# Performance work log

Hardware: AMD Instinct MI355X
Metric: run time of the kernel (lower is better)

Reference implementation:

```python
import jax, jax.numpy as jnp
import numpy as np

B, S, V, NB = 4, 2048, 50257, 32
TEMPERATURE = 0.07
TAU = 1.0  # F.gumbel_softmax default tau


def setup_inputs() -> dict:
    key = jax.random.key(0)
    k_ids, k_proto, k_gumbel = jax.random.split(key, 3)
    token_ids = jax.random.randint(k_ids, (B, S), 0, V)
    onehot_tokens = jax.nn.one_hot(token_ids, V, dtype=jnp.float32)  # [B,S,V]
    prototypes = jax.random.normal(k_proto, (NB, V), dtype=jnp.float32)
    # Gumbel(0,1) noise, pre-sampled so the reference is deterministic
    u = jax.random.uniform(k_gumbel, (B, S, NB), dtype=jnp.float32,
                           minval=1e-20, maxval=1.0)
    gumbel_noise = -jnp.log(-jnp.log(u))
    return {"onehot_tokens": onehot_tokens, "prototypes": prototypes,
            "gumbel_noise": gumbel_noise}


def reference(onehot_tokens, prototypes, gumbel_noise):
    # sims = onehot @ prototypes.T  (functionally a row gather) -> [B,S,NB]
    sims = jnp.einsum("bsv,nv->bsn", onehot_tokens, prototypes)
    logits = sims / TEMPERATURE
    # gumbel_softmax(hard=True): soft probs then straight-through hard one-hot
    y_soft = jax.nn.softmax((logits + gumbel_noise) / TAU, axis=-1)
    idx = jnp.argmax(y_soft, axis=-1)
    y_hard = jax.nn.one_hot(idx, NB, dtype=y_soft.dtype)
    out = y_hard - jax.lax.stop_gradient(y_soft) + y_soft
    return out
```

## Files before the change

kernel.cpp:

```cpp
#include <hip/hip_runtime.h>

#define B_    4
#define S_    2048
#define V_    50257
#define NB_   32
#define BS_   (B_ * S_)
static_assert((long long)BS_ * V_ % 4 == 0, "flat onehot must be float4-divisible");

__global__ __launch_bounds__(256) void find_tokens_kernel(
    const float4* __restrict__ onehot4, long long n4, int* __restrict__ tid)
{
    long long i = (long long)blockIdx.x * blockDim.x + threadIdx.x;
    long long stride = (long long)gridDim.x * blockDim.x;
    for (; i < n4; i += stride) {
        float4 v = onehot4[i];
        if (v.x != 0.0f || v.y != 0.0f || v.z != 0.0f || v.w != 0.0f) {
            long long base = i * 4;
            float vals[4] = {v.x, v.y, v.z, v.w};
            #pragma unroll
            for (int k = 0; k < 4; ++k) {
                if (vals[k] != 0.0f) {
                    long long idx = base + k;
                    int row = (int)(idx / V_);
                    int col = (int)(idx - (long long)row * V_);
                    tid[row] = col;
                }
            }
        }
    }
}

__global__ __launch_bounds__(256) void gumbel_hard_kernel(
    const float* __restrict__ proto,
    const float* __restrict__ gumbel,
    const int*   __restrict__ tid,
    float*       __restrict__ out)
{
    int row = blockIdx.x * blockDim.x + threadIdx.x;
    if (row >= BS_) return;
    int t = tid[row];

    float g[NB_];
    {
        const float4* g4 = reinterpret_cast<const float4*>(gumbel + (long long)row * NB_);
        #pragma unroll
        for (int q = 0; q < NB_ / 4; ++q) {
            float4 v = g4[q];
            g[q * 4 + 0] = v.x; g[q * 4 + 1] = v.y;
            g[q * 4 + 2] = v.z; g[q * 4 + 3] = v.w;
        }
    }

    float z[NB_];
    float m = -1e30f;
    int   am = 0;
    #pragma unroll
    for (int n = 0; n < NB_; ++n) {
        float s = proto[(long long)n * V_ + t];
        float zn = s / 0.07f + g[n];
        z[n] = zn;
        if (zn > m) { m = zn; am = n; }
    }

    float e[NB_];
    float sum = 0.0f;
    #pragma unroll
    for (int n = 0; n < NB_; ++n) {
        e[n] = __expf(z[n] - m);
        sum += e[n];
    }
    float inv = 1.0f / sum;

    float4* o4 = reinterpret_cast<float4*>(out + (long long)row * NB_);
    #pragma unroll
    for (int q = 0; q < NB_ / 4; ++q) {
        float4 v;
        float r[4];
        #pragma unroll
        for (int k = 0; k < 4; ++k) {
            int n = q * 4 + k;
            float y = e[n] * inv;
            float h = (n == am) ? 1.0f : 0.0f;
            r[k] = (h - y) + y;
        }
        v.x = r[0]; v.y = r[1]; v.z = r[2]; v.w = r[3];
        o4[q] = v;
    }
}

extern "C" void kernel_launch(void* const* d_in, const int* in_sizes, int n_in,
                              void* d_out, int out_size, void* d_ws, size_t ws_size,
                              hipStream_t stream)
{
    const float* onehot = (const float*)d_in[0];
    const float* proto  = (const float*)d_in[1];
    const float* gumbel = (const float*)d_in[2];
    float* out = (float*)d_out;
    int* tid = (int*)d_ws;

    long long n4 = ((long long)BS_ * V_) / 4;

    find_tokens_kernel<<<4096, 256, 0, stream>>>(
        reinterpret_cast<const float4*>(onehot), n4, tid);

    gumbel_hard_kernel<<<(BS_ + 255) / 256, 256, 0, stream>>>(
        proto, gumbel, tid, out);
}
```

Measured before the change: 299.9 us.

## Fuse token scan and gumbel-hard emission into a single streaming kernel

Merges the one-hot scan and the per-row softmax/argmax kernels into one kernel: the thread that finds a nonzero element computes and writes that row's output directly, so the tid workspace and the second launch go away. The scan loop is unrolled four-way to keep more loads in flight, the nonzero test uses integer bit checks, and the grid drops from 4096 to 2048 blocks. The emission work becomes divergent inside scanning wavefronts, but it is rare compared with the memory-bound scan of about 1.6 GB.

```diff
diff --git a/kernel.cpp b/kernel.cpp
--- a/kernel.cpp
+++ b/kernel.cpp
@@ -5,41 +5,16 @@
 #define V_    50257
 #define NB_   32
 #define BS_   (B_ * S_)
+#define TEMP_ 0.07f
+
 static_assert((long long)BS_ * V_ % 4 == 0, "flat onehot must be float4-divisible");
 
-__global__ __launch_bounds__(256) void find_tokens_kernel(
-    const float4* __restrict__ onehot4, long long n4, int* __restrict__ tid)
-{
-    long long i = (long long)blockIdx.x * blockDim.x + threadIdx.x;
-    long long stride = (long long)gridDim.x * blockDim.x;
-    for (; i < n4; i += stride) {
-        float4 v = onehot4[i];
-        if (v.x != 0.0f || v.y != 0.0f || v.z != 0.0f || v.w != 0.0f) {
-            long long base = i * 4;
-            float vals[4] = {v.x, v.y, v.z, v.w};
-            #pragma unroll
-            for (int k = 0; k < 4; ++k) {
-                if (vals[k] != 0.0f) {
-                    long long idx = base + k;
-                    int row = (int)(idx / V_);
-                    int col = (int)(idx - (long long)row * V_);
-                    tid[row] = col;
-                }
-            }
-        }
-    }
-}
-
-__global__ __launch_bounds__(256) void gumbel_hard_kernel(
+__device__ __forceinline__ void emit_row(
+    int row, int t,
     const float* __restrict__ proto,
     const float* __restrict__ gumbel,
-    const int*   __restrict__ tid,
     float*       __restrict__ out)
 {
-    int row = blockIdx.x * blockDim.x + threadIdx.x;
-    if (row >= BS_) return;
-    int t = tid[row];
-
     float g[NB_];
     {
         const float4* g4 = reinterpret_cast<const float4*>(gumbel + (long long)row * NB_);
@@ -57,7 +32,7 @@
     #pragma unroll
     for (int n = 0; n < NB_; ++n) {
         float s = proto[(long long)n * V_ + t];
-        float zn = s / 0.07f + g[n];
+        float zn = s / TEMP_ + g[n];
         z[n] = zn;
         if (zn > m) { m = zn; am = n; }
     }
@@ -74,8 +49,7 @@
     float4* o4 = reinterpret_cast<float4*>(out + (long long)row * NB_);
     #pragma unroll
     for (int q = 0; q < NB_ / 4; ++q) {
-        float4 v;
-        float r[4];
+        float4 v; float r[4];
         #pragma unroll
         for (int k = 0; k < 4; ++k) {
             int n = q * 4 + k;
@@ -88,6 +62,53 @@
     }
 }
 
+__device__ __forceinline__ void check_vec(
+    float4 v, long long idx4,
+    const float* __restrict__ proto, const float* __restrict__ gumbel,
+    float* __restrict__ out)
+{
+    int4 u = *reinterpret_cast<int4*>(&v);
+    if (__builtin_expect((u.x | u.y | u.z | u.w) != 0, 0)) {
+        long long base = idx4 * 4;
+        #pragma unroll
+        for (int k = 0; k < 4; ++k) {
+            int uk = (k == 0) ? u.x : (k == 1) ? u.y : (k == 2) ? u.z : u.w;
+            if (uk != 0) {
+                long long idx = base + k;
+                int row = (int)(idx / V_);
+                int col = (int)(idx - (long long)row * V_);
+                emit_row(row, col, proto, gumbel, out);
+            }
+        }
+    }
+}
+
+__global__ __launch_bounds__(256) void fused_scan_kernel(
+    const float4* __restrict__ onehot4,
+    const float*  __restrict__ proto,
+    const float*  __restrict__ gumbel,
+    float*        __restrict__ out)
+{
+    const long long n4 = (long long)BS_ * V_ / 4;
+    const long long stride = (long long)gridDim.x * blockDim.x;
+    long long i = (long long)blockIdx.x * blockDim.x + threadIdx.x;
+
+    for (; i + 3 * stride < n4; i += 4 * stride) {
+        float4 a = onehot4[i];
+        float4 b = onehot4[i + stride];
+        float4 c = onehot4[i + 2 * stride];
+        float4 d = onehot4[i + 3 * stride];
+        check_vec(a, i,              proto, gumbel, out);
+        check_vec(b, i + stride,     proto, gumbel, out);
+        check_vec(c, i + 2 * stride, proto, gumbel, out);
+        check_vec(d, i + 3 * stride, proto, gumbel, out);
+    }
+    for (; i < n4; i += stride) {
+        float4 a = onehot4[i];
+        check_vec(a, i, proto, gumbel, out);
+    }
+}
+
 extern "C" void kernel_launch(void* const* d_in, const int* in_sizes, int n_in,
                               void* d_out, int out_size, void* d_ws, size_t ws_size,
                               hipStream_t stream)
@@ -96,13 +117,7 @@
     const float* proto  = (const float*)d_in[1];
     const float* gumbel = (const float*)d_in[2];
     float* out = (float*)d_out;
-    int* tid = (int*)d_ws;
 
-    long long n4 = ((long long)BS_ * V_) / 4;
-
-    find_tokens_kernel<<<4096, 256, 0, stream>>>(
-        reinterpret_cast<const float4*>(onehot), n4, tid);
-
-    gumbel_hard_kernel<<<(BS_ + 255) / 256, 256, 0, stream>>>(
-        proto, gumbel, tid, out);
+    fused_scan_kernel<<<2048, 256, 0, stream>>>(
+        reinterpret_cast<const float4*>(onehot), proto, gumbel, out);
 }
```

Result: slower. 367.8 us (+22.7%).
